# Optimization experiments

Hardware: AMD Instinct MI355X
Metric: run time of the kernel (lower is better)

The kernel has to match this reference:

```python
import jax, jax.numpy as jnp
import numpy as np

B, T, DIM, HEADS = 8, 2048, 1024, 16
HD = DIM // HEADS


def setup_inputs() -> dict:
    key = jax.random.key(0)
    ks = jax.random.split(key, 12)
    s = 0.02
    z = jnp.zeros((DIM,), jnp.float32)
    return {
        "x": jax.random.normal(ks[0], (B, T, DIM), jnp.float32),
        "Wq": jax.random.normal(ks[1], (DIM, DIM), jnp.float32) * s,
        "bq": z,
        "Wk": jax.random.normal(ks[2], (DIM, DIM), jnp.float32) * s,
        "bk": z,
        "Wv": jax.random.normal(ks[3], (DIM, DIM), jnp.float32) * s,
        "bv": z,
        "w_rwkv": jax.random.normal(ks[4], (HEADS, HD), jnp.float32) * 0.5,
        "u_rwkv": jax.random.normal(ks[5], (HEADS, HD), jnp.float32) * 0.5,
        "Wo": jax.random.normal(ks[6], (DIM, DIM), jnp.float32) * s,
        "bo": z,
    }


def reference(x, Wq, bq, Wk, bk, Wv, bv, w_rwkv, u_rwkv, Wo, bo):
    N, T_, _ = x.shape
    # queries are computed but never used in the original forward
    _ = x @ Wq + bq
    k = (x @ Wk + bk).reshape(N, T_, HEADS, HD)
    v = (x @ Wv + bv).reshape(N, T_, HEADS, HD)
    kt = jnp.moveaxis(k, 1, 0)  # [T, N, H, D]
    vt = jnp.moveaxis(v, 1, 0)  # [T, N, H, D]

    u = u_rwkv  # [H, D] broadcasts against [N, H, D]
    w = w_rwkv

    def step(carry, kv):
        pp, aa, bb = carry
        k_t, v_t = kv
        # output at step t (with bonus u)
        ww = u + k_t
        qq = jnp.maximum(ww, pp)
        e1 = jnp.exp(pp - qq)
        e2 = jnp.exp(ww - qq)
        o_t = (e1 * aa + e2 * v_t) / (e1 * bb + e2)
        # state update (with decay w)
        ww2 = pp - w
        qq2 = jnp.maximum(ww2, k_t)
        e1b = jnp.exp(ww2 - qq2)
        e2b = jnp.exp(k_t - qq2)
        aa2 = e1b * aa + e2b * v_t
        bb2 = e1b * bb + e2b
        return (qq2, aa2, bb2), o_t

    init = (kt[0], vt[0], jnp.ones_like(kt[0]))  # pp, aa, bb
    _, o_rest = jax.lax.scan(step, init, (kt[1:], vt[1:]))  # [T-1, N, H, D]
    O = jnp.concatenate([vt[:1], o_rest], axis=0)  # O[0] = v[0]
    O = jnp.moveaxis(O, 0, 1).reshape(N, T_, -1)  # [N, T, dim]
    return O @ Wo + bo
```

## Files before the change

kernel.cpp:

```cpp
#include <hip/hip_runtime.h>

#define DIMSZ 1024
#define NB 8
#define TSEQ 2048
#define MTOT (NB*TSEQ)
#define CCH 64
#define LCH (TSEQ/CCH)
#define NCHAN (NB*DIMSZ)

typedef __attribute__((ext_vector_type(8))) short short8v;
typedef __attribute__((ext_vector_type(4))) float f32x4;

__device__ __forceinline__ unsigned short f2bf(float f) {
  unsigned int u; __builtin_memcpy(&u, &f, 4);
  unsigned int r = u + 0x7FFF + ((u >> 16) & 1);
  return (unsigned short)(r >> 16);
}
__device__ __forceinline__ float bf2f(unsigned short us) {
  unsigned int v = ((unsigned int)us) << 16;
  float f; __builtin_memcpy(&f, &v, 4); return f;
}

__device__ __forceinline__ void gload16(const void* g, void* l) {
  __builtin_amdgcn_global_load_lds(
      (const __attribute__((address_space(1))) void*)g,
      (__attribute__((address_space(3))) void*)l, 16, 0, 0);
}

__global__ __launch_bounds__(256) void cast_x_kernel(
    const float* __restrict__ in, unsigned short* __restrict__ out) {
  int i = blockIdx.x * 256 + threadIdx.x;
  float4 f = reinterpret_cast<const float4*>(in)[i];
  uint2 o;
  o.x = (unsigned)f2bf(f.x) | ((unsigned)f2bf(f.y) << 16);
  o.y = (unsigned)f2bf(f.z) | ((unsigned)f2bf(f.w) << 16);
  reinterpret_cast<uint2*>(out)[i] = o;
}

__global__ __launch_bounds__(256) void transpose_cast_kernel(
    const float* __restrict__ W, unsigned short* __restrict__ WT) {
  __shared__ float tile[32][33];
  int tx = threadIdx.x & 31, ty = threadIdx.x >> 5;
  int row0 = blockIdx.y * 32, col0 = blockIdx.x * 32;
  #pragma unroll
  for (int j = 0; j < 32; j += 8)
    tile[ty + j][tx] = W[(size_t)(row0 + ty + j) * DIMSZ + col0 + tx];
  __syncthreads();
  #pragma unroll
  for (int j = 0; j < 32; j += 8)
    WT[(size_t)(col0 + ty + j) * DIMSZ + row0 + tx] = f2bf(tile[tx][ty + j]);
}


#define VM2 asm volatile("s_waitcnt vmcnt(2)" ::: "memory")
#define VM0 asm volatile("s_waitcnt vmcnt(0)" ::: "memory")

#define PH_BAR do {                         \
  __builtin_amdgcn_s_barrier();             \
  __builtin_amdgcn_sched_barrier(0);        \
} while(0)

#define STAGE(BUF, OP, HALF, T) do {                                        \
  const unsigned short* _s = (OP) ? BT : Aop;                               \
  const int _rb = ((OP) ? bcol : brow) + (HALF)*128 + wid*16;               \
  char* _lb = smem + (BUF)*65536 + (OP)*32768 + ((HALF)*128 + wid*16)*128;  \
  const size_t _k0 = (size_t)(T)*64;                                        \
  gload16(&_s[(size_t)(_rb + srow)*K + _k0 + (sg^srow)*8], _lb);            \
  gload16(&_s[(size_t)(_rb + 8 + srow)*K + _k0 + (sg^srow)*8], _lb + 1024); \
} while(0)

#define READ_A(DST, BUF, MH) do {                                           \
  _Pragma("unroll")                                                         \
  for (int _m = 0; _m < 4; ++_m) {                                          \
    const char* _pa = smem + (BUF)*65536 +                                  \
        ((MH)*128 + wr*64 + _m*16 + lrow)*128;                              \
    DST[_m][0] = *(const short8v*)(_pa + ((lko*2) ^ rds));                  \
    DST[_m][1] = *(const short8v*)(_pa + (((32+lko)*2) ^ rds));             \
  }                                                                         \
} while(0)

#define READ_B(DST, BUF, NH) do {                                           \
  _Pragma("unroll")                                                         \
  for (int _n = 0; _n < 2; ++_n) {                                          \
    const char* _pb = smem + (BUF)*65536 + 32768 +                          \
        ((NH)*128 + wc*32 + _n*16 + lrow)*128;                              \
    DST[_n][0] = *(const short8v*)(_pb + ((lko*2) ^ rds));                  \
    DST[_n][1] = *(const short8v*)(_pb + (((32+lko)*2) ^ rds));             \
  }                                                                         \
} while(0)

#define MFMA_Q(MH, NH, AF, BF) do {                                         \
  __builtin_amdgcn_s_setprio(1);                                            \
  _Pragma("unroll")                                                         \
  for (int _m = 0; _m < 4; ++_m)                                            \
    _Pragma("unroll")                                                       \
    for (int _n = 0; _n < 2; ++_n) {                                        \
      acc[(MH)*4+_m][(NH)*2+_n] = __builtin_amdgcn_mfma_f32_16x16x32_bf16(  \
          AF[_m][0], BF[_n][0], acc[(MH)*4+_m][(NH)*2+_n], 0, 0, 0);        \
      acc[(MH)*4+_m][(NH)*2+_n] = __builtin_amdgcn_mfma_f32_16x16x32_bf16(  \
          AF[_m][1], BF[_n][1], acc[(MH)*4+_m][(NH)*2+_n], 0, 0, 0);        \
    }                                                                       \
  __builtin_amdgcn_s_setprio(0);                                            \
} while(0)

template<int OUTBF>
__global__ __launch_bounds__(512) void gemm256_kernel(
    const unsigned short* __restrict__ Aop,
    const unsigned short* __restrict__ BT,
    void* __restrict__ Cv,
    const float* __restrict__ bias0,
    const float* __restrict__ bias1,
    int M, int N, int K, int Nsplit) {
  extern __shared__ char smem[];
  const int tid  = threadIdx.x;
  const int wid  = tid >> 6;
  const int lane = tid & 63;
  const int wr   = wid >> 2;
  const int wc   = wid & 3;
  const int brow = blockIdx.x * 256;
  const int bcol = blockIdx.y * 256;
  const int lrow = lane & 15;
  const int lko  = (lane >> 4) * 8;
  const int rds  = (lrow & 7) << 4;
  const int srow = lane >> 3;
  const int sg   = lane & 7;

  f32x4 acc[8][4];
  #pragma unroll
  for (int m = 0; m < 8; ++m)
    #pragma unroll
    for (int n = 0; n < 4; ++n)
      acc[m][n] = (f32x4){0.f, 0.f, 0.f, 0.f};

  short8v a0[4][2], a1[4][2], bf0[2][2], bf1[2][2];

  STAGE(0, 0, 0, 0);
  STAGE(0, 1, 0, 0);
  STAGE(0, 1, 1, 0);
  STAGE(0, 0, 1, 0);
  VM2;
  PH_BAR;
  READ_A(a0, 0, 0); READ_B(bf0, 0, 0);

  const int NT = K >> 6;
  for (int t = 0; t < NT - 1; ++t) {
    const int b = t & 1, nb = b ^ 1;
    READ_B(bf1, b, 1);
    STAGE(nb, 0, 0, t + 1); VM2; PH_BAR;
    MFMA_Q(0, 0, a0, bf0); PH_BAR;
    READ_A(a1, b, 1);
    STAGE(nb, 1, 0, t + 1); PH_BAR;
    MFMA_Q(0, 1, a0, bf1); PH_BAR;
    STAGE(nb, 1, 1, t + 1); VM2; PH_BAR;
    MFMA_Q(1, 0, a1, bf0); PH_BAR;
    READ_A(a0, nb, 0); READ_B(bf0, nb, 0);
    STAGE(nb, 0, 1, t + 1); VM2; PH_BAR;
    MFMA_Q(1, 1, a1, bf1); PH_BAR;
  }
  {
    const int b = (NT - 1) & 1;
    READ_B(bf1, b, 1);
    VM0; PH_BAR;
    MFMA_Q(0, 0, a0, bf0);
    READ_A(a1, b, 1);
    MFMA_Q(0, 1, a0, bf1);
    MFMA_Q(1, 0, a1, bf0);
    MFMA_Q(1, 1, a1, bf1);
  }

  #pragma unroll
  for (int mf = 0; mf < 8; ++mf) {
    const int rowb = brow + (mf >= 4) * 128 + wr * 64 + (mf & 3) * 16 + (lane >> 4) * 4;
    #pragma unroll
    for (int nf = 0; nf < 4; ++nf) {
      const int col = bcol + (nf >= 2) * 128 + wc * 32 + (nf & 1) * 16 + lrow;
      const float bb = (col < Nsplit) ? bias0[col] : bias1[col - Nsplit];
      #pragma unroll
      for (int r = 0; r < 4; ++r) {
        const float val = acc[mf][nf][r] + bb;
        if (OUTBF) {
          ((unsigned short*)Cv)[(size_t)(rowb + r) * N + col] = f2bf(val);
        } else {
          ((float*)Cv)[(size_t)(rowb + r) * N + col] = val;
        }
      }
    }
  }
}


__device__ __forceinline__ void wkv_step(float& p, float& a, float& b,
                                         float kt, float vt, float w) {
  float ww2 = p - w;
  float qq2 = fmaxf(ww2, kt);
  float e1 = __expf(ww2 - qq2);
  float e2 = __expf(kt - qq2);
  a = e1 * a + e2 * vt;
  b = e1 * b + e2;
  p = qq2;
}

__global__ __launch_bounds__(256) void wkv_chunk_state_kernel(
    const unsigned short* __restrict__ kv,
    const float* __restrict__ wdec,
    float* __restrict__ stP, float* __restrict__ stA, float* __restrict__ stB) {
  int idx = blockIdx.x * 256 + threadIdx.x;
  int cp = idx & 511;
  int n = (idx >> 9) & (NB - 1);
  int chunk = idx >> 12;
  int c = cp * 2;
  float2 w2 = *reinterpret_cast<const float2*>(&wdec[c]);
  const unsigned short* base = kv + (size_t)(n * TSEQ + chunk * LCH) * 2048 + c;
  float p0 = -1e30f, a0 = 0.f, b0 = 0.f;
  float p1 = -1e30f, a1 = 0.f, b1 = 0.f;
  #pragma unroll 8
  for (int j = 0; j < LCH; ++j) {
    unsigned int kk = *reinterpret_cast<const unsigned int*>(&base[(size_t)j * 2048]);
    unsigned int vv = *reinterpret_cast<const unsigned int*>(&base[(size_t)j * 2048 + 1024]);
    wkv_step(p0, a0, b0, bf2f(kk & 0xffff), bf2f(vv & 0xffff), w2.x);
    wkv_step(p1, a1, b1, bf2f(kk >> 16),    bf2f(vv >> 16),    w2.y);
  }
  int soff = chunk * NCHAN + n * 1024 + c;
  *reinterpret_cast<float2*>(&stP[soff]) = make_float2(p0, p1);
  *reinterpret_cast<float2*>(&stA[soff]) = make_float2(a0, a1);
  *reinterpret_cast<float2*>(&stB[soff]) = make_float2(b0, b1);
}

__global__ __launch_bounds__(256) void wkv_scan_kernel(
    const float* __restrict__ wdec,
    float* __restrict__ stP, float* __restrict__ stA, float* __restrict__ stB) {
  int idx = blockIdx.x * 256 + threadIdx.x;
  int c = idx & 1023;
  float decay = (float)LCH * wdec[c];
  float p = -1e30f, a = 0.f, b = 0.f;
  for (int i = 0; i < CCH; ++i) {
    int off = i * NCHAN + idx;
    float pc = stP[off], ac = stA[off], bc = stB[off];
    stP[off] = p; stA[off] = a; stB[off] = b;
    float pd = p - decay;
    float q = fmaxf(pd, pc);
    float e1 = __expf(pd - q);
    float e2 = __expf(pc - q);
    a = e1 * a + e2 * ac;
    b = e1 * b + e2 * bc;
    p = q;
  }
}

__global__ __launch_bounds__(256) void wkv_out_kernel(
    const unsigned short* __restrict__ kv,
    const float* __restrict__ wdec, const float* __restrict__ ubon,
    const float* __restrict__ stP, const float* __restrict__ stA,
    const float* __restrict__ stB,
    unsigned short* __restrict__ O) {
  int idx = blockIdx.x * 256 + threadIdx.x;
  int cp = idx & 511;
  int n = (idx >> 9) & (NB - 1);
  int chunk = idx >> 12;
  int c = cp * 2;
  float2 w2 = *reinterpret_cast<const float2*>(&wdec[c]);
  float2 u2 = *reinterpret_cast<const float2*>(&ubon[c]);
  const unsigned short* base = kv + (size_t)(n * TSEQ + chunk * LCH) * 2048 + c;
  unsigned short* ob = O + (size_t)(n * TSEQ + chunk * LCH) * DIMSZ + c;
  int soff = chunk * NCHAN + n * 1024 + c;
  float2 pP = *reinterpret_cast<const float2*>(&stP[soff]);
  float2 pA = *reinterpret_cast<const float2*>(&stA[soff]);
  float2 pB = *reinterpret_cast<const float2*>(&stB[soff]);
  float p0 = pP.x, a0 = pA.x, b0 = pB.x;
  float p1 = pP.y, a1 = pA.y, b1 = pB.y;
  #pragma unroll 4
  for (int j = 0; j < LCH; ++j) {
    unsigned int kk = *reinterpret_cast<const unsigned int*>(&base[(size_t)j * 2048]);
    unsigned int vv = *reinterpret_cast<const unsigned int*>(&base[(size_t)j * 2048 + 1024]);
    float k0 = bf2f(kk & 0xffff), k1 = bf2f(kk >> 16);
    float v0 = bf2f(vv & 0xffff), v1 = bf2f(vv >> 16);
    float ww0 = u2.x + k0, ww1 = u2.y + k1;
    float qq0 = fmaxf(ww0, p0), qq1 = fmaxf(ww1, p1);
    float e10 = __expf(p0 - qq0), e20 = __expf(ww0 - qq0);
    float e11 = __expf(p1 - qq1), e21 = __expf(ww1 - qq1);
    float o0 = (e10 * a0 + e20 * v0) * __builtin_amdgcn_rcpf(e10 * b0 + e20);
    float o1 = (e11 * a1 + e21 * v1) * __builtin_amdgcn_rcpf(e11 * b1 + e21);
    *reinterpret_cast<unsigned int*>(&ob[(size_t)j * DIMSZ]) =
        (unsigned)f2bf(o0) | ((unsigned)f2bf(o1) << 16);
    wkv_step(p0, a0, b0, k0, v0, w2.x);
    wkv_step(p1, a1, b1, k1, v1, w2.y);
  }
}

extern "C" void kernel_launch(void* const* d_in, const int* in_sizes, int n_in,
                              void* d_out, int out_size, void* d_ws, size_t ws_size,
                              hipStream_t stream) {
  const float* x  = (const float*)d_in[0];
  const float* Wk = (const float*)d_in[3];
  const float* bk = (const float*)d_in[4];
  const float* Wv = (const float*)d_in[5];
  const float* bv = (const float*)d_in[6];
  const float* wr = (const float*)d_in[7];
  const float* ur = (const float*)d_in[8];
  const float* Wo = (const float*)d_in[9];
  const float* bo = (const float*)d_in[10];
  float* out = (float*)d_out;

  char* ws = (char*)d_ws;
  unsigned short* xb   = (unsigned short*)(ws);
  unsigned short* WTkv = (unsigned short*)(ws + 33554432);
  unsigned short* WoT  = (unsigned short*)(ws + 37748736);
  unsigned short* kvb  = (unsigned short*)(ws + 39845888);

  float* stP = out;
  float* stA = out + CCH * NCHAN;
  float* stB = out + 2 * CCH * NCHAN;

  cast_x_kernel<<<dim3(16384), dim3(256), 0, stream>>>(x, xb);
  transpose_cast_kernel<<<dim3(32, 32), dim3(256), 0, stream>>>(Wk, WTkv);
  transpose_cast_kernel<<<dim3(32, 32), dim3(256), 0, stream>>>(Wv, WTkv + 1024 * 1024);
  transpose_cast_kernel<<<dim3(32, 32), dim3(256), 0, stream>>>(Wo, WoT);

  gemm256_kernel<1><<<dim3(64, 8), dim3(512), 131072, stream>>>(
      xb, WTkv, (void*)kvb, bk, bv, MTOT, 2048, 1024, 1024);

  wkv_chunk_state_kernel<<<dim3(CCH * NB * 512 / 256), dim3(256), 0, stream>>>(
      kvb, wr, stP, stA, stB);
  wkv_scan_kernel<<<dim3(NCHAN / 256), dim3(256), 0, stream>>>(wr, stP, stA, stB);
  wkv_out_kernel<<<dim3(CCH * NB * 512 / 256), dim3(256), 0, stream>>>(
      kvb, wr, ur, stP, stA, stB, xb);

  gemm256_kernel<0><<<dim3(64, 4), dim3(512), 131072, stream>>>(
      xb, WoT, (void*)out, bo, bo, MTOT, 1024, 1024, 1024);
}
```

Measured before the change: 169.1 us.

## Deepen GEMM prefetch to two k-tiles ahead with finer LDS/VMEM waits

Restructures the bf16 MFMA GEMM main loop so global-to-LDS staging runs two k-tiles ahead instead of one. Each quarter of the current tile now has its own explicit lgkmcnt waits, and the vmcnt threshold is raised to 6. The prologue stages one and three-quarter tiles up front, and the separate epilogue iteration is folded into the loop with guards. The aim is to hide global load latency better, at the cost of more barriers per iteration and a tighter ordering on LDS buffer reuse.

Result: slower. 177.4 us (+4.9%).

```diff
diff --git a/kernel.cpp b/kernel.cpp
--- a/kernel.cpp
+++ b/kernel.cpp
@@ -52,12 +52,16 @@
 }
 
 
-#define VM2 asm volatile("s_waitcnt vmcnt(2)" ::: "memory")
-#define VM0 asm volatile("s_waitcnt vmcnt(0)" ::: "memory")
-
-#define PH_BAR do {                         \
-  __builtin_amdgcn_s_barrier();             \
-  __builtin_amdgcn_sched_barrier(0);        \
+#define VM6    asm volatile("s_waitcnt vmcnt(6)" ::: "memory")
+#define VM0    asm volatile("s_waitcnt vmcnt(0)" ::: "memory")
+#define LGKM8  asm volatile("s_waitcnt lgkmcnt(8)" ::: "memory")
+#define LGKM0SGB do {                                         \
+  asm volatile("s_waitcnt lgkmcnt(0)" ::: "memory");          \
+  __builtin_amdgcn_sched_barrier(0);                          \
+} while(0)
+#define BAR do {                                              \
+  __builtin_amdgcn_s_barrier();                               \
+  __builtin_amdgcn_sched_barrier(0);                          \
 } while(0)
 
 #define STAGE(BUF, OP, HALF, T) do {                                        \
@@ -134,38 +138,32 @@
 
   short8v a0[4][2], a1[4][2], bf0[2][2], bf1[2][2];
 
-  STAGE(0, 0, 0, 0);
-  STAGE(0, 1, 0, 0);
-  STAGE(0, 1, 1, 0);
-  STAGE(0, 0, 1, 0);
-  VM2;
-  PH_BAR;
-  READ_A(a0, 0, 0); READ_B(bf0, 0, 0);
+  STAGE(0, 0, 0, 0); STAGE(0, 1, 0, 0); STAGE(0, 1, 1, 0); STAGE(0, 0, 1, 0);
+  STAGE(1, 0, 0, 1); STAGE(1, 1, 0, 1); STAGE(1, 1, 1, 1);
+  VM6;
+  BAR;
 
   const int NT = K >> 6;
-  for (int t = 0; t < NT - 1; ++t) {
+  for (int t = 0; t < NT; ++t) {
     const int b = t & 1, nb = b ^ 1;
+    const bool s1 = (t + 1 < NT), s2 = (t + 2 < NT);
+    READ_A(a0, b, 0); READ_B(bf0, b, 0);
+    if (s1) STAGE(nb, 0, 1, t + 1);
+    LGKM8;
+    BAR; LGKM0SGB;
+    MFMA_Q(0, 0, a0, bf0); BAR;
     READ_B(bf1, b, 1);
-    STAGE(nb, 0, 0, t + 1); VM2; PH_BAR;
-    MFMA_Q(0, 0, a0, bf0); PH_BAR;
+    if (s2) STAGE(b, 0, 0, t + 2);
+    BAR; LGKM0SGB;
+    MFMA_Q(0, 1, a0, bf1); BAR;
     READ_A(a1, b, 1);
-    STAGE(nb, 1, 0, t + 1); PH_BAR;
-    MFMA_Q(0, 1, a0, bf1); PH_BAR;
-    STAGE(nb, 1, 1, t + 1); VM2; PH_BAR;
-    MFMA_Q(1, 0, a1, bf0); PH_BAR;
-    READ_A(a0, nb, 0); READ_B(bf0, nb, 0);
-    STAGE(nb, 0, 1, t + 1); VM2; PH_BAR;
-    MFMA_Q(1, 1, a1, bf1); PH_BAR;
-  }
-  {
-    const int b = (NT - 1) & 1;
-    READ_B(bf1, b, 1);
-    VM0; PH_BAR;
-    MFMA_Q(0, 0, a0, bf0);
-    READ_A(a1, b, 1);
-    MFMA_Q(0, 1, a0, bf1);
-    MFMA_Q(1, 0, a1, bf0);
-    MFMA_Q(1, 1, a1, bf1);
+    if (s2) STAGE(b, 1, 0, t + 2);
+    BAR; LGKM0SGB;
+    MFMA_Q(1, 0, a1, bf0); BAR;
+    if (s2) { STAGE(b, 1, 1, t + 2); VM6; }
+    else if (s1) { VM0; }
+    BAR;
+    MFMA_Q(1, 1, a1, bf1); BAR;
   }
 
   #pragma unroll
```
